# Kernel tuning notes

Hardware: AMD Instinct MI355X
Metric: run time of the kernel (lower is better)

Reference implementation:

```python
import jax, jax.numpy as jnp
import numpy as np


def setup_inputs() -> dict:
    key = jax.random.key(0)
    ks = jax.random.split(key, 9)
    B, C, H, W = 16, 512, 64, 64
    s = 1.0 / np.sqrt(C)  # fan-in style init scale for 1x1 conv weights
    x = jax.random.normal(ks[0], (B, C, H, W), dtype=jnp.float32)
    W_theta = jax.random.normal(ks[1], (C, C), dtype=jnp.float32) * s
    b_theta = jax.random.normal(ks[2], (C,), dtype=jnp.float32) * 0.01
    W_phi = jax.random.normal(ks[3], (C, C), dtype=jnp.float32) * s
    b_phi = jax.random.normal(ks[4], (C,), dtype=jnp.float32) * 0.01
    W_g = jax.random.normal(ks[5], (C, C), dtype=jnp.float32) * s
    b_g = jax.random.normal(ks[6], (C,), dtype=jnp.float32) * 0.01
    W_out = jax.random.normal(ks[7], (C, C), dtype=jnp.float32) * s
    b_out = jax.random.normal(ks[8], (C,), dtype=jnp.float32) * 0.01
    return {
        "x": x,
        "W_theta": W_theta, "b_theta": b_theta,
        "W_phi": W_phi, "b_phi": b_phi,
        "W_g": W_g, "b_g": b_g,
        "W_out": W_out, "b_out": b_out,
    }


def reference(x, W_theta, b_theta, W_phi, b_phi, W_g, b_g, W_out, b_out):
    B, C, H, W = x.shape
    n = H * W
    xf = x.reshape(B, C, n)  # [B, C, HW]

    def conv1x1(Wm, b):
        # 1x1 conv == channel-mixing GEMM: [O,C] x [B,C,N] -> [B,O,N]
        return jnp.einsum('oc,bcn->bon', Wm, xf) + b[None, :, None]

    phi = conv1x1(W_phi, b_phi)      # [B, C, HW]
    theta = conv1x1(W_theta, b_theta)  # [B, C, HW] (used transposed: 'b (h w) c')
    g = conv1x1(W_g, b_g)            # [B, C, HW]

    # phi @ theta^T over spatial dim -> [B, C, C] channel-channel attention
    scores = jnp.einsum('bcn,bdn->bcd', phi, theta) * (1.0 / C)
    attn = jax.nn.softmax(scores, axis=2)  # softmax over last (dim=2), as in torch
    Y = jnp.einsum('bcd,bdn->bcn', attn, g)  # [B, C, HW]

    A = jnp.einsum('oc,bcn->bon', W_out, Y) + b_out[None, :, None]
    return x + A.reshape(B, C, H, W)
```

## Files before the change

kernel.cpp:

```cpp
#include <hip/hip_runtime.h>
#include <hip/hip_bf16.h>
#include <stdint.h>


typedef unsigned short u16;
typedef __attribute__((ext_vector_type(8))) short frag8;
typedef __attribute__((ext_vector_type(4))) float f32x4;

__device__ __forceinline__ u16 f2bf(float f) {
  union { __hip_bfloat16 h; u16 u; } c; c.h = __float2bfloat16(f); return c.u;
}

__device__ __forceinline__ void gl_lds16(const u16* g, u16* l) {
  __builtin_amdgcn_global_load_lds(
      (const __attribute__((address_space(1))) void*)g,
      (__attribute__((address_space(3))) void*)l, 16, 0, 0);
}

#define SCHED0 __builtin_amdgcn_sched_barrier(0)
#define SBAR   __builtin_amdgcn_s_barrier()

__global__ __launch_bounds__(256) void prep_x(const float* __restrict__ X,
                                              u16* __restrict__ XT,
                                              u16* __restrict__ XB,
                                              float* __restrict__ S) {
  const int b = blockIdx.z;
  const int n0 = blockIdx.x * 64;
  const int c0 = blockIdx.y * 64;
  __shared__ u16 t[64][72];
  const float* Xb = X + (int64_t)b * (512LL * 4096);
  const int tid = threadIdx.x;
  const int r = tid >> 3;
  const int e8 = (tid & 7) * 8;

  const float* p0 = Xb + (int64_t)(c0 + r) * 4096 + n0 + e8;
  const float* p1 = p0 + 32LL * 4096;
  const float4 f0 = *(const float4*)(p0);
  const float4 f1 = *(const float4*)(p0 + 4);
  const float4 h0 = *(const float4*)(p1);
  const float4 h1 = *(const float4*)(p1 + 4);

  union { uint4 q; u16 u[8]; } pa, pb;
  pa.u[0] = f2bf(f0.x); pa.u[1] = f2bf(f0.y); pa.u[2] = f2bf(f0.z); pa.u[3] = f2bf(f0.w);
  pa.u[4] = f2bf(f1.x); pa.u[5] = f2bf(f1.y); pa.u[6] = f2bf(f1.z); pa.u[7] = f2bf(f1.w);
  pb.u[0] = f2bf(h0.x); pb.u[1] = f2bf(h0.y); pb.u[2] = f2bf(h0.z); pb.u[3] = f2bf(h0.w);
  pb.u[4] = f2bf(h1.x); pb.u[5] = f2bf(h1.y); pb.u[6] = f2bf(h1.z); pb.u[7] = f2bf(h1.w);

  const int rowA = r, rowB = r + 32;
  *(uint4*)(XB + ((int64_t)b * 512 + c0 + rowA) * 4096 + n0 + e8) = pa.q;
  *(uint4*)(XB + ((int64_t)b * 512 + c0 + rowB) * 4096 + n0 + e8) = pb.q;
  *(uint4*)&t[rowA][e8 ^ (rowA & 56)] = pa.q;
  *(uint4*)&t[rowB][e8 ^ (rowB & 56)] = pb.q;

  float sa = f0.x + f0.y + f0.z + f0.w + f1.x + f1.y + f1.z + f1.w;
  float sb = h0.x + h0.y + h0.z + h0.w + h1.x + h1.y + h1.z + h1.w;
  sa += __shfl_xor(sa, 1); sa += __shfl_xor(sa, 2); sa += __shfl_xor(sa, 4);
  sb += __shfl_xor(sb, 1); sb += __shfl_xor(sb, 2); sb += __shfl_xor(sb, 4);
  if ((tid & 7) == 0) {
    atomicAdd(&S[b * 512 + c0 + rowA], sa);
    atomicAdd(&S[b * 512 + c0 + rowB], sb);
  }
  __syncthreads();
#pragma unroll
  for (int p = 0; p < 2; p++) {
    const int nr = p * 32 + r;
    union { uint4 q; u16 u[8]; } o;
#pragma unroll
    for (int j = 0; j < 8; j++)
      o.u[j] = t[e8 + j][nr ^ e8];
    *(uint4*)(XT + ((int64_t)b * 4096 + n0 + nr) * 512 + c0 + e8) = o.q;
  }
}

__constant__ const int g_ty[10] = {0,0,0,0,1,1,1,2,2,3};
__constant__ const int g_tx[10] = {0,1,2,3,1,2,3,2,3,3};

__global__ __launch_bounds__(256) void gram_sk(const u16* __restrict__ XB,
                                               u16* __restrict__ G) {
  const int flat = blockIdx.x;
  const int w = (flat & 7) * 20 + (flat >> 3);
  const int b = w / 10;
  const int tl = w - b * 10;
  const int m0 = g_ty[tl] * 128, n0 = g_tx[tl] * 128;
  const int tid = threadIdx.x;
  const int lane = tid & 63, wave = tid >> 6;
  __shared__ u16 sA[3][8192];
  __shared__ u16 sB[3][8192];
  const u16* Xb = XB + (int64_t)b * (512LL * 4096);

  f32x4 acc[4][4];
#pragma unroll
  for (int i = 0; i < 4; i++)
#pragma unroll
    for (int j = 0; j < 4; j++)
#pragma unroll
      for (int r = 0; r < 4; r++) acc[i][j][r] = 0.0f;

  const int fr = lane & 15;
  const int hi = lane >> 4;
  const int fkx0 = ((hi) ^ (fr & 7)) * 8;
  const int fkx1 = ((4 + hi) ^ (fr & 7)) * 8;
  const int wm = (wave & 1) * 64, wn = (wave >> 1) * 64;

  const int srow = tid >> 3;
  const int scol = (((tid & 7) ^ ((tid >> 3) & 7))) * 8;
  const u16* ArA = Xb + (int64_t)(m0 + srow) * 4096 + scol;
  const u16* BrA = Xb + (int64_t)(n0 + srow) * 4096 + scol;

  auto stage = [&](int t, int buf) {
    const u16* a = ArA + t * 64;
    const u16* bb = BrA + t * 64;
#pragma unroll
    for (int d = 0; d < 4; d++) {
      gl_lds16(a + (int64_t)d * (32 * 4096), sA[buf] + d * 2048 + tid * 8);
      gl_lds16(bb + (int64_t)d * (32 * 4096), sB[buf] + d * 2048 + tid * 8);
    }
  };
  auto comp = [&](int buf) {
#pragma unroll
    for (int kk = 0; kk < 2; kk++) {
      const int fx = kk ? fkx1 : fkx0;
      frag8 af[4], bf[4];
#pragma unroll
      for (int i = 0; i < 4; i++) {
        af[i] = *(const frag8*)(sA[buf] + (wm + i * 16 + fr) * 64 + fx);
        bf[i] = *(const frag8*)(sB[buf] + (wn + i * 16 + fr) * 64 + fx);
      }
#pragma unroll
      for (int i = 0; i < 4; i++)
#pragma unroll
        for (int j = 0; j < 4; j++)
          acc[i][j] = __builtin_amdgcn_mfma_f32_16x16x32_bf16(af[i], bf[j], acc[i][j], 0, 0, 0);
    }
  };

  stage(0, 0); stage(1, 1);
  for (int t = 0; t < 62; t++) {
    SCHED0; SBAR; SCHED0;
    stage(t + 2, (t + 2) % 3);
    asm volatile("s_waitcnt vmcnt(16)" ::: "memory");
    SBAR; SCHED0;
    comp(t % 3);
  }
  asm volatile("s_waitcnt vmcnt(0)" ::: "memory");
  SBAR; SCHED0;
  comp(62 % 3); comp(63 % 3);

  u16* Gb = G + (int64_t)b * 262144;
  const int quad = lane >> 4;
#pragma unroll
  for (int i = 0; i < 4; i++)
#pragma unroll
    for (int j = 0; j < 4; j++) {
      const int row0 = m0 + wm + i * 16 + quad * 4;
      const int col = n0 + wn + j * 16 + fr;
      union { u16 u[4]; uint2 v; } mg;
#pragma unroll
      for (int r = 0; r < 4; r++) {
        const u16 h = f2bf(acc[i][j][r]);
        Gb[(int64_t)(row0 + r) * 512 + col] = h;
        mg.u[r] = h;
      }
      if (m0 != n0)
        *(uint2*)(Gb + (int64_t)col * 512 + row0) = mg.v;
    }
}

enum { EPI_BF16 = 0, EPI_SCORES = 1, EPI_BF16I = 2 };

template <int EPI>
__global__ __launch_bounds__(256) void gemm128_bt(
    const u16* __restrict__ A, int64_t sAb, int lda,
    const u16* __restrict__ B, int64_t sBb, int ldb,
    void* __restrict__ Cv, int64_t sCb, int ldc,
    const float* __restrict__ e_bphi, const float* __restrict__ e_btheta,
    const float* __restrict__ e_uphi, const float* __restrict__ e_utheta) {
  const int flat = blockIdx.x;
  const int w = (flat & 7) * 32 + (flat >> 3);
  const int b = w >> 4;
  const int rem = w & 15;
  const int m0 = (rem >> 2) * 128, n0 = (rem & 3) * 128;
  const int tid = threadIdx.x;
  const int lane = tid & 63, wave = tid >> 6;
  __shared__ u16 sA[4][4096];
  __shared__ u16 sB[4][4096];
  const u16* Ab = A + (int64_t)b * sAb;
  const u16* Bb = B + (int64_t)b * sBb;

  f32x4 acc[4][4];
#pragma unroll
  for (int i = 0; i < 4; i++)
#pragma unroll
    for (int j = 0; j < 4; j++)
#pragma unroll
      for (int r = 0; r < 4; r++) acc[i][j][r] = 0.0f;

  const int srow = tid >> 2;
  const int scol = (((tid & 3) ^ ((tid >> 3) & 3))) * 8;
  const int fr = lane & 15;
  const int fkx = (((lane >> 4) ^ ((fr >> 1) & 3))) * 8;
  const int wm = (wave & 1) * 64, wn = (wave >> 1) * 64;

  const u16* Ar0 = Ab + (int64_t)(m0 + srow) * lda + scol;
  const u16* Ar1 = Ab + (int64_t)(m0 + 64 + srow) * lda + scol;
  const u16* Br0 = Bb + (int64_t)(n0 + srow) * ldb + scol;
  const u16* Br1 = Bb + (int64_t)(n0 + 64 + srow) * ldb + scol;

  auto stage = [&](int t, int buf) {
    gl_lds16(Ar0 + t * 32, sA[buf] + tid * 8);
    gl_lds16(Ar1 + t * 32, sA[buf] + 2048 + tid * 8);
    gl_lds16(Br0 + t * 32, sB[buf] + tid * 8);
    gl_lds16(Br1 + t * 32, sB[buf] + 2048 + tid * 8);
  };
  auto comp = [&](int buf) {
    frag8 af[4], bf[4];
#pragma unroll
    for (int i = 0; i < 4; i++) {
      af[i] = *(const frag8*)(sA[buf] + (wm + i * 16 + fr) * 32 + fkx);
      bf[i] = *(const frag8*)(sB[buf] + (wn + i * 16 + fr) * 32 + fkx);
    }
#pragma unroll
    for (int i = 0; i < 4; i++)
#pragma unroll
      for (int j = 0; j < 4; j++)
        acc[i][j] = __builtin_amdgcn_mfma_f32_16x16x32_bf16(af[i], bf[j], acc[i][j], 0, 0, 0);
  };

  stage(0, 0); stage(1, 1); stage(2, 2);
#pragma unroll
  for (int t = 0; t < 13; t++) {
    SCHED0; SBAR; SCHED0;
    stage(t + 3, (t + 3) % 4);
    asm volatile("s_waitcnt vmcnt(12)" ::: "memory");
    SBAR; SCHED0;
    comp(t % 4);
  }
  asm volatile("s_waitcnt vmcnt(8)" ::: "memory");
  SBAR; SCHED0;
  comp(13 % 4);
  asm volatile("s_waitcnt vmcnt(4)" ::: "memory");
  SBAR; SCHED0;
  comp(14 % 4);
  asm volatile("s_waitcnt vmcnt(0)" ::: "memory");
  SBAR; SCHED0;
  comp(15 % 4);

  const int quad = lane >> 4;
#pragma unroll
  for (int i = 0; i < 4; i++)
#pragma unroll
    for (int j = 0; j < 4; j++)
#pragma unroll
      for (int r = 0; r < 4; r++) {
        const int row = m0 + wm + i * 16 + quad * 4 + r;
        const int col = n0 + wn + j * 16 + fr;
        const float a = acc[i][j][r];
        if constexpr (EPI == EPI_BF16) {
          ((u16*)Cv)[(int64_t)b * sCb + (int64_t)row * ldc + col] = f2bf(a);
        } else if constexpr (EPI == EPI_BF16I) {
          ((u16*)Cv)[(int64_t)b * sCb + (int64_t)row * ldc + col] =
              f2bf(a + (row == col ? 1.0f : 0.0f));
        } else {
          const float bp = e_bphi[row];
          const float bt = e_btheta[col];
          ((float*)Cv)[(int64_t)b * sCb + (int64_t)row * ldc + col] =
              (a + bp * e_utheta[b * 512 + col] + bt * e_uphi[b * 512 + row] +
               4096.0f * bp * bt) * (1.0f / 512.0f);
        }
      }
}

__global__ __launch_bounds__(256) void gemm_final(const u16* __restrict__ M,
                                                  const u16* __restrict__ XT,
                                                  const float* __restrict__ V,
                                                  float* __restrict__ O) {
  const int flat = blockIdx.x;
  const int w = (flat & 7) * 256 + (flat >> 3);
  const int b = w >> 7;
  const int rem = w & 127;
  const int m0 = (rem >> 5) * 128;
  const int n0 = (rem & 31) * 128;
  const int tid = threadIdx.x;
  const int lane = tid & 63, wave = tid >> 6;
  __shared__ u16 sA[2][4096];
  __shared__ u16 sB[2][4096];
  const u16* Ab = M + (int64_t)b * 262144;
  const u16* Bb = XT + (int64_t)b * (4096LL * 512);

  f32x4 acc[4][4];
#pragma unroll
  for (int i = 0; i < 4; i++)
#pragma unroll
    for (int j = 0; j < 4; j++)
#pragma unroll
      for (int r = 0; r < 4; r++) acc[i][j][r] = 0.0f;

  const int srow = tid >> 2;
  const int scol = (((tid & 3) ^ ((tid >> 3) & 3))) * 8;
  const int fr = lane & 15;
  const int fkx = (((lane >> 4) ^ ((fr >> 1) & 3))) * 8;
  const int wm = (wave & 1) * 64, wn = (wave >> 1) * 64;

  const u16* Ar0 = Ab + (int64_t)(m0 + srow) * 512 + scol;
  const u16* Ar1 = Ab + (int64_t)(m0 + 64 + srow) * 512 + scol;
  const u16* Br0 = Bb + (int64_t)(n0 + srow) * 512 + scol;
  const u16* Br1 = Bb + (int64_t)(n0 + 64 + srow) * 512 + scol;

  gl_lds16(Ar0, sA[0] + tid * 8);
  gl_lds16(Ar1, sA[0] + 2048 + tid * 8);
  gl_lds16(Br0, sB[0] + tid * 8);
  gl_lds16(Br1, sB[0] + 2048 + tid * 8);
  __syncthreads();

  for (int k0 = 0; k0 < 512; k0 += 32) {
    const int cur = (k0 >> 5) & 1;
    if (k0 + 32 < 512) {
      u16* dA = sA[cur ^ 1];
      u16* dB = sB[cur ^ 1];
      gl_lds16(Ar0 + k0 + 32, dA + tid * 8);
      gl_lds16(Ar1 + k0 + 32, dA + 2048 + tid * 8);
      gl_lds16(Br0 + k0 + 32, dB + tid * 8);
      gl_lds16(Br1 + k0 + 32, dB + 2048 + tid * 8);
    }
    frag8 af[4], bf[4];
#pragma unroll
    for (int i = 0; i < 4; i++) {
      af[i] = *(const frag8*)(sA[cur] + (wm + i * 16 + fr) * 32 + fkx);
      bf[i] = *(const frag8*)(sB[cur] + (wn + i * 16 + fr) * 32 + fkx);
    }
#pragma unroll
    for (int i = 0; i < 4; i++)
#pragma unroll
      for (int j = 0; j < 4; j++)
        acc[i][j] = __builtin_amdgcn_mfma_f32_16x16x32_bf16(af[i], bf[j], acc[i][j], 0, 0, 0);
    __syncthreads();
  }

  const int quad = lane >> 4;
#pragma unroll
  for (int i = 0; i < 4; i++)
#pragma unroll
    for (int j = 0; j < 4; j++)
#pragma unroll
      for (int r = 0; r < 4; r++) {
        const int row = m0 + wm + i * 16 + quad * 4 + r;
        const int col = n0 + wn + j * 16 + fr;
        O[(int64_t)b * (512LL * 4096) + (int64_t)row * 4096 + col] =
            acc[i][j][r] + V[b * 512 + row];
      }
}

__global__ __launch_bounds__(256) void uv_kernel(const float* __restrict__ Wphi,
                                                 const float* __restrict__ Wtheta,
                                                 const float* __restrict__ S,
                                                 float* __restrict__ UPH, float* __restrict__ UTH) {
  const int b = blockIdx.x;
  const int o0 = blockIdx.y * 64;
  const int tid = threadIdx.x;
  __shared__ float s[512];
  s[tid] = S[b * 512 + tid];
  s[tid + 256] = S[b * 512 + tid + 256];
  __syncthreads();
  const int o = o0 + (tid >> 2);
  const int q = tid & 3;
  float a0 = 0.f, a1 = 0.f;
  for (int c = q * 128; c < q * 128 + 128; c += 4) {
    const float4 wa = *(const float4*)(Wphi + (int64_t)o * 512 + c);
    const float4 wb = *(const float4*)(Wtheta + (int64_t)o * 512 + c);
    a0 += wa.x * s[c] + wa.y * s[c + 1] + wa.z * s[c + 2] + wa.w * s[c + 3];
    a1 += wb.x * s[c] + wb.y * s[c + 1] + wb.z * s[c + 2] + wb.w * s[c + 3];
  }
  a0 += __shfl_xor(a0, 1); a0 += __shfl_xor(a0, 2);
  a1 += __shfl_xor(a1, 1); a1 += __shfl_xor(a1, 2);
  if (q == 0) {
    UPH[b * 512 + o] = a0;
    UTH[b * 512 + o] = a1;
  }
}

__global__ __launch_bounds__(256) void v_kernel(const float* __restrict__ Wout,
                                                const float* __restrict__ R,
                                                const float* __restrict__ bout,
                                                float* __restrict__ V) {
  const int b = blockIdx.x;
  const int o0 = blockIdx.y * 64;
  const int tid = threadIdx.x;
  __shared__ float s[512];
  s[tid] = R[b * 512 + tid];
  s[tid + 256] = R[b * 512 + tid + 256];
  __syncthreads();
  const int o = o0 + (tid >> 2);
  const int q = tid & 3;
  float a0 = 0.f;
  for (int c = q * 128; c < q * 128 + 128; c += 4) {
    const float4 wa = *(const float4*)(Wout + (int64_t)o * 512 + c);
    a0 += wa.x * s[c] + wa.y * s[c + 1] + wa.z * s[c + 2] + wa.w * s[c + 3];
  }
  a0 += __shfl_xor(a0, 1); a0 += __shfl_xor(a0, 2);
  if (q == 0) V[b * 512 + o] = a0 + bout[o];
}

__global__ __launch_bounds__(256) void convert_w(const float* __restrict__ W0,
                                                 const float* __restrict__ W1,
                                                 const float* __restrict__ W2,
                                                 u16* __restrict__ O0, u16* __restrict__ O1,
                                                 u16* __restrict__ O2) {
  const int idx = blockIdx.x * 256 + threadIdx.x;
  const int m = idx >> 16;
  const int off = (idx & 65535) * 4;
  const float* src = (m == 0) ? W0 : (m == 1) ? W1 : W2;
  u16* dst = (m == 0) ? O0 : (m == 1) ? O1 : O2;
  const float4 f = *(const float4*)(src + off);
  union { u16 u[4]; uint2 v; } p;
  p.u[0] = f2bf(f.x); p.u[1] = f2bf(f.y); p.u[2] = f2bf(f.z); p.u[3] = f2bf(f.w);
  *(uint2*)(dst + off) = p.v;
}

__global__ void wg_transpose(const float* __restrict__ Wg, u16* __restrict__ WgT) {
  __shared__ float t[16][17];
  const int i0 = blockIdx.y * 16, j0 = blockIdx.x * 16;
  t[threadIdx.y][threadIdx.x] = Wg[(i0 + threadIdx.y) * 512 + j0 + threadIdx.x];
  __syncthreads();
  WgT[(j0 + threadIdx.y) * 512 + i0 + threadIdx.x] = f2bf(t[threadIdx.x][threadIdx.y]);
}

__global__ __launch_bounds__(64) void softmax_k(float* __restrict__ SC,
                                                const float* __restrict__ bg,
                                                float* __restrict__ R) {
  const int row = blockIdx.x;
  const int lane = threadIdx.x;
  float* Sr = SC + (int64_t)row * 512;
  union { float4 q[2]; float v[8]; } u;
  u.q[0] = *(const float4*)(Sr + lane * 8);
  u.q[1] = *(const float4*)(Sr + lane * 8 + 4);
  const float4 g0 = *(const float4*)(bg + lane * 8);
  const float4 g1 = *(const float4*)(bg + lane * 8 + 4);
  const float gb[8] = { g0.x, g0.y, g0.z, g0.w, g1.x, g1.y, g1.z, g1.w };
  float m = u.v[0];
#pragma unroll
  for (int j = 1; j < 8; j++) m = fmaxf(m, u.v[j]);
#pragma unroll
  for (int off = 32; off > 0; off >>= 1) m = fmaxf(m, __shfl_xor(m, off));
  float e[8], s = 0.f, sb = 0.f;
#pragma unroll
  for (int j = 0; j < 8; j++) {
    e[j] = __expf(u.v[j] - m);
    s += e[j];
    sb += e[j] * gb[j];
  }
#pragma unroll
  for (int off = 32; off > 0; off >>= 1) { s += __shfl_xor(s, off); sb += __shfl_xor(sb, off); }
  const float inv = 1.0f / s;
  union { uint4 q; u16 h[8]; } o;
#pragma unroll
  for (int j = 0; j < 8; j++) o.h[j] = f2bf(e[j] * inv);
  *(uint4*)((u16*)SC + (int64_t)row * 1024 + lane * 8) = o.q;
  if (lane == 0) R[row] = sb * inv;
}

extern "C" void kernel_launch(void* const* d_in, const int* in_sizes, int n_in,
                              void* d_out, int out_size, void* d_ws, size_t ws_size,
                              hipStream_t stream) {
  const float* x      = (const float*)d_in[0];
  const float* Wtheta = (const float*)d_in[1];
  const float* btheta = (const float*)d_in[2];
  const float* Wphi   = (const float*)d_in[3];
  const float* bphi   = (const float*)d_in[4];
  const float* Wg     = (const float*)d_in[5];
  const float* bg     = (const float*)d_in[6];
  const float* Wout   = (const float*)d_in[7];
  const float* bout   = (const float*)d_in[8];

  char* ws = (char*)d_ws;
  u16*   xT     = (u16*)(ws + 0);
  u16*   G      = (u16*)(ws + 67108864);
  u16*   T1     = (u16*)(ws + 75497472);
  float* SC     = (float*)(ws + 83886080);
  u16*   Wphib  = (u16*)(ws + 100663296);
  u16*   Wthetab= (u16*)(ws + 101187584);
  u16*   Woutb  = (u16*)(ws + 101711872);
  u16*   WgTb   = (u16*)(ws + 102236160);
  float* S      = (float*)(ws + 102760448);
  float* UPH    = (float*)(ws + 102793216);
  float* UTH    = (float*)(ws + 102825984);
  float* R      = (float*)(ws + 102858752);
  float* V      = (float*)(ws + 102891520);
  u16* ATT = (u16*)SC;
  u16* Q = G;
  u16* M = T1;

  u16*   XB = (u16*)d_out;

  hipMemsetAsync(S, 0, 32768, stream);
  prep_x<<<dim3(64, 8, 16), 256, 0, stream>>>(x, xT, XB, S);
  uv_kernel<<<dim3(16, 8), 256, 0, stream>>>(Wphi, Wtheta, S, UPH, UTH);
  convert_w<<<768, 256, 0, stream>>>(Wphi, Wtheta, Wout, Wphib, Wthetab, Woutb);
  wg_transpose<<<dim3(32, 32), dim3(16, 16), 0, stream>>>(Wg, WgTb);
  gram_sk<<<dim3(160), 256, 0, stream>>>(XB, G);
  gemm128_bt<EPI_BF16><<<dim3(256), 256, 0, stream>>>(
      Wphib, 0, 512, G, 512LL * 512, 512, T1, 512LL * 512, 512,
      nullptr, nullptr, nullptr, nullptr);
  gemm128_bt<EPI_SCORES><<<dim3(256), 256, 0, stream>>>(
      T1, 512LL * 512, 512, Wthetab, 0, 512, SC, 512LL * 512, 512,
      bphi, btheta, UPH, UTH);
  softmax_k<<<8192, 64, 0, stream>>>(SC, bg, R);
  gemm128_bt<EPI_BF16><<<dim3(256), 256, 0, stream>>>(
      WgTb, 0, 512, ATT, 512LL * 1024, 1024, Q, 512LL * 512, 512,
      nullptr, nullptr, nullptr, nullptr);
  gemm128_bt<EPI_BF16I><<<dim3(256), 256, 0, stream>>>(
      Woutb, 0, 512, Q, 512LL * 512, 512, M, 512LL * 512, 512,
      nullptr, nullptr, nullptr, nullptr);
  v_kernel<<<dim3(16, 8), 256, 0, stream>>>(Wout, R, bout, V);
  gemm_final<<<dim3(2048), 256, 0, stream>>>(M, xT, V, (float*)d_out);
}
```

Baseline: 446.2 us.

## Fuse scores GEMM with row softmax in a full-row-tile kernel

Replaces the separate scores GEMM (fp32 output) and softmax kernel with one kernel. Each block computes a 32x512 strip of scores, so it holds whole rows and can run the softmax in registers, reducing across waves through shared memory. This removes the fp32 score write and read-back plus one launch. In exchange the tiles are narrower and re-stream the full W_theta per block, and the 3-stage LDS buffers are large, which may lower occupancy.

```diff
diff --git a/kernel.cpp b/kernel.cpp
--- a/kernel.cpp
+++ b/kernel.cpp
@@ -166,15 +166,13 @@
     }
 }
 
-enum { EPI_BF16 = 0, EPI_SCORES = 1, EPI_BF16I = 2 };
+enum { EPI_BF16 = 0, EPI_BF16I = 2 };
 
 template <int EPI>
 __global__ __launch_bounds__(256) void gemm128_bt(
     const u16* __restrict__ A, int64_t sAb, int lda,
     const u16* __restrict__ B, int64_t sBb, int ldb,
-    void* __restrict__ Cv, int64_t sCb, int ldc,
-    const float* __restrict__ e_bphi, const float* __restrict__ e_btheta,
-    const float* __restrict__ e_uphi, const float* __restrict__ e_utheta) {
+    void* __restrict__ Cv, int64_t sCb, int ldc) {
   const int flat = blockIdx.x;
   const int w = (flat & 7) * 32 + (flat >> 3);
   const int b = w >> 4;
@@ -257,17 +255,193 @@
         const float a = acc[i][j][r];
         if constexpr (EPI == EPI_BF16) {
           ((u16*)Cv)[(int64_t)b * sCb + (int64_t)row * ldc + col] = f2bf(a);
-        } else if constexpr (EPI == EPI_BF16I) {
+        } else {
           ((u16*)Cv)[(int64_t)b * sCb + (int64_t)row * ldc + col] =
               f2bf(a + (row == col ? 1.0f : 0.0f));
-        } else {
-          const float bp = e_bphi[row];
-          const float bt = e_btheta[col];
-          ((float*)Cv)[(int64_t)b * sCb + (int64_t)row * ldc + col] =
-              (a + bp * e_utheta[b * 512 + col] + bt * e_uphi[b * 512 + row] +
-               4096.0f * bp * bt) * (1.0f / 512.0f);
         }
       }
+}
+
+__global__ __launch_bounds__(256) void scores_softmax(
+    const u16* __restrict__ T1, const u16* __restrict__ Wthetab,
+    const float* __restrict__ e_bphi, const float* __restrict__ e_btheta,
+    const float* __restrict__ e_uphi, const float* __restrict__ e_utheta,
+    const float* __restrict__ bg,
+    u16* __restrict__ ATT, float* __restrict__ R) {
+  const int flat = blockIdx.x;
+  const int w = (flat & 7) * 32 + (flat >> 3);
+  const int b = w >> 4;
+  const int m0 = (w & 15) * 32;
+  const int tid = threadIdx.x;
+  const int lane = tid & 63, wave = tid >> 6;
+  const int fr = lane & 15, quad = lane >> 4;
+  const int wn = wave * 128;
+
+  __shared__ u16 sA[3][1024];
+  __shared__ u16 sB[3][16384];
+  __shared__ float rmax[4][32], rsum[4][32], rsbg[4][32];
+
+  f32x4 acc[2][8];
+#pragma unroll
+  for (int i = 0; i < 2; i++)
+#pragma unroll
+    for (int j = 0; j < 8; j++)
+#pragma unroll
+      for (int r = 0; r < 4; r++) acc[i][j][r] = 0.0f;
+
+  const int srow = tid >> 2;
+  const int scol = (((tid & 3) ^ ((tid >> 3) & 3))) * 8;
+  const int fkx = (((lane >> 4) ^ ((fr >> 1) & 3))) * 8;
+
+  const u16* Ar = T1 + (int64_t)b * (512LL * 512) + (int64_t)(m0 + (srow & 31)) * 512 + scol;
+  const u16* Br = Wthetab + (int64_t)srow * 512 + scol;
+
+  auto stage = [&](int t, int buf) {
+    if (tid < 128)
+      gl_lds16(Ar + t * 32, sA[buf] + tid * 8);
+#pragma unroll
+    for (int d = 0; d < 8; d++)
+      gl_lds16(Br + (int64_t)d * (64 * 512) + t * 32, sB[buf] + d * 2048 + tid * 8);
+  };
+  auto comp = [&](int buf) {
+    frag8 af[2], bf[8];
+#pragma unroll
+    for (int i = 0; i < 2; i++)
+      af[i] = *(const frag8*)(sA[buf] + (i * 16 + fr) * 32 + fkx);
+#pragma unroll
+    for (int j = 0; j < 8; j++)
+      bf[j] = *(const frag8*)(sB[buf] + (wn + j * 16 + fr) * 32 + fkx);
+#pragma unroll
+    for (int i = 0; i < 2; i++)
+#pragma unroll
+      for (int j = 0; j < 8; j++)
+        acc[i][j] = __builtin_amdgcn_mfma_f32_16x16x32_bf16(af[i], bf[j], acc[i][j], 0, 0, 0);
+  };
+
+  stage(0, 0); stage(1, 1);
+#pragma unroll
+  for (int t = 0; t < 14; t++) {
+    SCHED0; SBAR; SCHED0;
+    stage(t + 2, (t + 2) % 3);
+    asm volatile("s_waitcnt vmcnt(16)" ::: "memory");
+    SBAR; SCHED0;
+    comp(t % 3);
+  }
+  asm volatile("s_waitcnt vmcnt(0)" ::: "memory");
+  SBAR; SCHED0;
+  comp(14 % 3); comp(15 % 3);
+
+  float bth[8], uthv[8], bgv[8];
+#pragma unroll
+  for (int j = 0; j < 8; j++) {
+    const int col = wn + j * 16 + fr;
+    bth[j] = e_btheta[col];
+    uthv[j] = e_utheta[b * 512 + col];
+    bgv[j] = bg[col];
+  }
+  float bph[2][4], uphv[2][4];
+#pragma unroll
+  for (int i = 0; i < 2; i++)
+#pragma unroll
+    for (int r = 0; r < 4; r++) {
+      const int grow = m0 + i * 16 + quad * 4 + r;
+      bph[i][r] = e_bphi[grow];
+      uphv[i][r] = e_uphi[b * 512 + grow];
+    }
+#pragma unroll
+  for (int i = 0; i < 2; i++)
+#pragma unroll
+    for (int j = 0; j < 8; j++)
+#pragma unroll
+      for (int r = 0; r < 4; r++)
+        acc[i][j][r] = (acc[i][j][r] + bph[i][r] * uthv[j] + bth[j] * uphv[i][r] +
+                        4096.0f * bph[i][r] * bth[j]) * (1.0f / 512.0f);
+
+  float m8[2][4];
+#pragma unroll
+  for (int i = 0; i < 2; i++)
+#pragma unroll
+    for (int r = 0; r < 4; r++) {
+      float m = acc[i][0][r];
+#pragma unroll
+      for (int j = 1; j < 8; j++) m = fmaxf(m, acc[i][j][r]);
+      m8[i][r] = m;
+    }
+#pragma unroll
+  for (int off = 1; off < 16; off <<= 1)
+#pragma unroll
+    for (int i = 0; i < 2; i++)
+#pragma unroll
+      for (int r = 0; r < 4; r++) m8[i][r] = fmaxf(m8[i][r], __shfl_xor(m8[i][r], off));
+  if (fr == 0)
+#pragma unroll
+    for (int i = 0; i < 2; i++)
+#pragma unroll
+      for (int r = 0; r < 4; r++) rmax[wave][i * 16 + quad * 4 + r] = m8[i][r];
+  __syncthreads();
+#pragma unroll
+  for (int i = 0; i < 2; i++)
+#pragma unroll
+    for (int r = 0; r < 4; r++) {
+      const int lr = i * 16 + quad * 4 + r;
+      float m = rmax[0][lr];
+#pragma unroll
+      for (int ww = 1; ww < 4; ww++) m = fmaxf(m, rmax[ww][lr]);
+      m8[i][r] = m;
+    }
+
+  float s8[2][4], g8[2][4];
+#pragma unroll
+  for (int i = 0; i < 2; i++)
+#pragma unroll
+    for (int r = 0; r < 4; r++) { s8[i][r] = 0.f; g8[i][r] = 0.f; }
+#pragma unroll
+  for (int i = 0; i < 2; i++)
+#pragma unroll
+    for (int j = 0; j < 8; j++)
+#pragma unroll
+      for (int r = 0; r < 4; r++) {
+        const float e = __expf(acc[i][j][r] - m8[i][r]);
+        acc[i][j][r] = e;
+        s8[i][r] += e;
+        g8[i][r] += e * bgv[j];
+      }
+#pragma unroll
+  for (int off = 1; off < 16; off <<= 1)
+#pragma unroll
+    for (int i = 0; i < 2; i++)
+#pragma unroll
+      for (int r = 0; r < 4; r++) {
+        s8[i][r] += __shfl_xor(s8[i][r], off);
+        g8[i][r] += __shfl_xor(g8[i][r], off);
+      }
+  if (fr == 0)
+#pragma unroll
+    for (int i = 0; i < 2; i++)
+#pragma unroll
+      for (int r = 0; r < 4; r++) {
+        const int lr = i * 16 + quad * 4 + r;
+        rsum[wave][lr] = s8[i][r];
+        rsbg[wave][lr] = g8[i][r];
+      }
+  __syncthreads();
+  u16* Ab = ATT + (int64_t)b * (512LL * 1024);
+#pragma unroll
+  for (int i = 0; i < 2; i++)
+#pragma unroll
+    for (int r = 0; r < 4; r++) {
+      const int lr = i * 16 + quad * 4 + r;
+      float tot = rsum[0][lr], gt = rsbg[0][lr];
+#pragma unroll
+      for (int ww = 1; ww < 4; ww++) { tot += rsum[ww][lr]; gt += rsbg[ww][lr]; }
+      const float inv = 1.0f / tot;
+      const int grow = m0 + lr;
+      if (wave == 0 && fr == 0) R[b * 512 + grow] = gt * inv;
+      u16* row = Ab + (int64_t)grow * 1024;
+#pragma unroll
+      for (int j = 0; j < 8; j++)
+        row[wn + j * 16 + fr] = f2bf(acc[i][j][r] * inv);
+    }
 }
 
 __global__ __launch_bounds__(256) void gemm_final(const u16* __restrict__ M,
@@ -424,40 +598,6 @@
   WgT[(j0 + threadIdx.y) * 512 + i0 + threadIdx.x] = f2bf(t[threadIdx.x][threadIdx.y]);
 }
 
-__global__ __launch_bounds__(64) void softmax_k(float* __restrict__ SC,
-                                                const float* __restrict__ bg,
-                                                float* __restrict__ R) {
-  const int row = blockIdx.x;
-  const int lane = threadIdx.x;
-  float* Sr = SC + (int64_t)row * 512;
-  union { float4 q[2]; float v[8]; } u;
-  u.q[0] = *(const float4*)(Sr + lane * 8);
-  u.q[1] = *(const float4*)(Sr + lane * 8 + 4);
-  const float4 g0 = *(const float4*)(bg + lane * 8);
-  const float4 g1 = *(const float4*)(bg + lane * 8 + 4);
-  const float gb[8] = { g0.x, g0.y, g0.z, g0.w, g1.x, g1.y, g1.z, g1.w };
-  float m = u.v[0];
-#pragma unroll
-  for (int j = 1; j < 8; j++) m = fmaxf(m, u.v[j]);
-#pragma unroll
-  for (int off = 32; off > 0; off >>= 1) m = fmaxf(m, __shfl_xor(m, off));
-  float e[8], s = 0.f, sb = 0.f;
-#pragma unroll
-  for (int j = 0; j < 8; j++) {
-    e[j] = __expf(u.v[j] - m);
-    s += e[j];
-    sb += e[j] * gb[j];
-  }
-#pragma unroll
-  for (int off = 32; off > 0; off >>= 1) { s += __shfl_xor(s, off); sb += __shfl_xor(sb, off); }
-  const float inv = 1.0f / s;
-  union { uint4 q; u16 h[8]; } o;
-#pragma unroll
-  for (int j = 0; j < 8; j++) o.h[j] = f2bf(e[j] * inv);
-  *(uint4*)((u16*)SC + (int64_t)row * 1024 + lane * 8) = o.q;
-  if (lane == 0) R[row] = sb * inv;
-}
-
 extern "C" void kernel_launch(void* const* d_in, const int* in_sizes, int n_in,
                               void* d_out, int out_size, void* d_ws, size_t ws_size,
                               hipStream_t stream) {
@@ -498,18 +638,13 @@
   wg_transpose<<<dim3(32, 32), dim3(16, 16), 0, stream>>>(Wg, WgTb);
   gram_sk<<<dim3(160), 256, 0, stream>>>(XB, G);
   gemm128_bt<EPI_BF16><<<dim3(256), 256, 0, stream>>>(
-      Wphib, 0, 512, G, 512LL * 512, 512, T1, 512LL * 512, 512,
-      nullptr, nullptr, nullptr, nullptr);
-  gemm128_bt<EPI_SCORES><<<dim3(256), 256, 0, stream>>>(
-      T1, 512LL * 512, 512, Wthetab, 0, 512, SC, 512LL * 512, 512,
-      bphi, btheta, UPH, UTH);
-  softmax_k<<<8192, 64, 0, stream>>>(SC, bg, R);
+      Wphib, 0, 512, G, 512LL * 512, 512, T1, 512LL * 512, 512);
+  scores_softmax<<<dim3(256), 256, 0, stream>>>(
+      T1, Wthetab, bphi, btheta, UPH, UTH, bg, ATT, R);
   gemm128_bt<EPI_BF16><<<dim3(256), 256, 0, stream>>>(
-      WgTb, 0, 512, ATT, 512LL * 1024, 1024, Q, 512LL * 512, 512,
-      nullptr, nullptr, nullptr, nullptr);
+      WgTb, 0, 512, ATT, 512LL * 1024, 1024, Q, 512LL * 512, 512);
   gemm128_bt<EPI_BF16I><<<dim3(256), 256, 0, stream>>>(
-      Woutb, 0, 512, Q, 512LL * 512, 512, M, 512LL * 512, 512,
-      nullptr, nullptr, nullptr, nullptr);
+      Woutb, 0, 512, Q, 512LL * 512, 512, M, 512LL * 512, 512);
   v_kernel<<<dim3(16, 8), 256, 0, stream>>>(Wout, R, bout, V);
   gemm_final<<<dim3(2048), 256, 0, stream>>>(M, xT, V, (float*)d_out);
 }
```

New measurement: 447.9 us. About the same (+0.4%).
